# Kernel optimization log

Measured on AMD Instinct MI355X. Metric: run time of the kernel, lower is better.

The kernel has to match this reference:

```python
import jax, jax.numpy as jnp
import numpy as np

K = 3  # n_components (hardcoded in original fit())
NORM = float(np.sqrt((2.0 * np.pi) ** 3))


def _prob(X, mean, dev):
    # X: [N,H,W,3], mean: [K,H,W,3], dev: [K,H,W] -> prob [N,K,H,W]
    d2 = jnp.sum(jnp.square(X[:, None] - mean[None]), axis=-1)  # [N,K,H,W]
    return jnp.exp(-d2 / (2.0 * jnp.square(dev)[None])) / (NORM * dev[None])


def _fit(frames, n_iter):
    N, H, W, _ = frames.shape
    # init: mean[k] = (k+1)/4, deviation = 1, weight = 1/K (as in original)
    mean = jnp.stack([jnp.full((H, W, 3), (k + 1) / 4.0, jnp.float32) for k in range(K)])
    dev = jnp.ones((K, H, W), jnp.float32)
    weight = jnp.full((K, H, W), 1.0 / K, jnp.float32)

    def step(carry, _):
        weight, mean, dev = carry
        P = _prob(frames, mean, dev)                      # [N,K,H,W]
        R = weight[None] * P
        R = R / jnp.sum(R, axis=1, keepdims=True)         # responsibilities
        Rs = jnp.sum(R, axis=0)                           # [K,H,W]
        w = Rs / N
        m = jnp.einsum('nkhw,nhwc->khwc', R, frames) / Rs[..., None]
        d = jnp.sum(R * jnp.sum(jnp.square(frames[:, None] - m[None]), axis=-1), axis=0) / Rs
        return (w, m, d), None

    (weight, mean, dev), _ = jax.lax.scan(step, (weight, mean, dev), None, length=n_iter)
    ratio = weight / dev
    fg = ratio <= jnp.min(ratio, axis=0)                  # [K,H,W] bool
    return weight, mean, dev, fg


def _process(frame, mean, dev, fg):
    # frame: [H,W,3]
    dist = jnp.sqrt(jnp.sum(jnp.square(frame[None] - mean), axis=-1))  # [K,H,W]
    index = jnp.argmin(dist, axis=0)                                   # [H,W]
    min_dist = jnp.min(dist, axis=0)                                   # [H,W]
    dev_c = jnp.take_along_axis(dev, index[None], axis=0)[0]
    mask1 = min_dist < dev_c * 2.5
    mask2 = jnp.take_along_axis(fg, index[None], axis=0)[0]
    _ = jnp.logical_and(mask1, mask2)  # computed but unused in original return
    # channel 0: original return (mask2 * 255); channel 1: min_dist (differentiable core)
    return jnp.stack([mask2.astype(jnp.float32) * 255.0, min_dist], axis=0)


def setup_inputs() -> dict:
    key = jax.random.key(0)
    k1, k2 = jax.random.split(key)
    frames = jax.random.uniform(k1, (8, 480, 640, 3), dtype=jnp.float32)
    frame = jax.random.uniform(k2, (480, 640, 3), dtype=jnp.float32)
    return {"frames": frames, "frame": frame, "n_iter": 5}


def reference(frames, frame, n_iter):
    weight, mean, dev, fg = _fit(frames, n_iter)
    return _process(frame, mean, dev, fg)
```

## Files before the change

kernel.cpp:

```cpp
#include <hip/hip_runtime.h>
#include <math.h>

#define KC 3
#define NF 8
#define NPJ 4
#define HH 480
#define WW 640
#define HWPIX (HH * WW)
#define FSTRIDE (HWPIX * 3)

typedef float v2f __attribute__((ext_vector_type(2)));

__device__ __forceinline__ float frcp(float x) { return __builtin_amdgcn_rcpf(x); }
__device__ __forceinline__ float fexp2(float x) { return __builtin_amdgcn_exp2f(x); }
__device__ __forceinline__ v2f exp2v(v2f x) { return (v2f){fexp2(x.x), fexp2(x.y)}; }
__device__ __forceinline__ v2f v2(float s) { return (v2f){s, s}; }

__global__ __launch_bounds__(64, 4) void gmm_fit_process_kernel(
    const float* __restrict__ frames,
    const float* __restrict__ frame,
    const int* __restrict__ n_iter_p,
    float* __restrict__ out)
{
    const int p = blockIdx.x * blockDim.x + threadIdx.x;
    if (p >= HWPIX) return;
    const int n_iter = *n_iter_p;

    v2f Xp[NPJ][3], X2p[NPJ];
#pragma unroll
    for (int j = 0; j < NPJ; ++j) {
        const float* s0 = frames + (size_t)(2 * j)     * FSTRIDE + (size_t)p * 3;
        const float* s1 = frames + (size_t)(2 * j + 1) * FSTRIDE + (size_t)p * 3;
        Xp[j][0] = (v2f){s0[0], s1[0]};
        Xp[j][1] = (v2f){s0[1], s1[1]};
        Xp[j][2] = (v2f){s0[2], s1[2]};
        X2p[j] = Xp[j][0] * Xp[j][0] + Xp[j][1] * Xp[j][1] + Xp[j][2] * Xp[j][2];
    }

    float mean[KC][3], dev[KC], weight[KC];
#pragma unroll
    for (int k = 0; k < KC; ++k) {
        const float m0 = (float)(k + 1) / 4.0f;
        mean[k][0] = m0; mean[k][1] = m0; mean[k][2] = m0;
        dev[k] = 1.0f;
        weight[k] = 1.0f / 3.0f;
    }

    const float INV_NORM = 0.06349363593424097f;
    const float L2E = 1.4426950408889634f;
    const float DEV_FLOOR = 1e-12f;
    const float S_FLOOR = 1e-20f;

    for (int it = 0; it < n_iter; ++it) {
        float A[KC], B[KC], C[KC], cc[KC];
#pragma unroll
        for (int k = 0; k < KC; ++k) {
            const float invd = frcp(fmaxf(dev[k], DEV_FLOOR));
            const float a2 = -0.5f * L2E * invd * invd;
            const float m2 = mean[k][0] * mean[k][0] + mean[k][1] * mean[k][1]
                           + mean[k][2] * mean[k][2];
            A[k] = a2;
            B[k] = a2 * m2;
            C[k] = -2.0f * a2;
            cc[k] = weight[k] * INV_NORM * invd;
        }

        v2f rs[KC], mx[KC], my[KC], mz[KC], ac2[KC];
#pragma unroll
        for (int k = 0; k < KC; ++k) {
            rs[k] = v2(0.0f); mx[k] = v2(0.0f); my[k] = v2(0.0f);
            mz[k] = v2(0.0f); ac2[k] = v2(0.0f);
        }

#pragma unroll
        for (int j = 0; j < NPJ; ++j) {
            v2f r[KC], s = v2(0.0f);
#pragma unroll
            for (int k = 0; k < KC; ++k) {
                const v2f t = v2(mean[k][0]) * Xp[j][0]
                            + v2(mean[k][1]) * Xp[j][1]
                            + v2(mean[k][2]) * Xp[j][2];
                v2f e = v2(A[k]) * X2p[j] + v2(B[k]);
                e = v2(C[k]) * t + e;
                r[k] = v2(cc[k]) * exp2v(e);
                s += r[k];
            }
            const v2f sinv = (v2f){ (s.x > S_FLOOR) ? frcp(s.x) : 0.0f,
                                    (s.y > S_FLOOR) ? frcp(s.y) : 0.0f };
#pragma unroll
            for (int k = 0; k < KC; ++k) {
                const v2f rk = r[k] * sinv;
                rs[k]  += rk;
                mx[k]  += rk * Xp[j][0];
                my[k]  += rk * Xp[j][1];
                mz[k]  += rk * Xp[j][2];
                ac2[k] += rk * X2p[j];
            }
        }

#pragma unroll
        for (int k = 0; k < KC; ++k) {
            const float rsk = rs[k].x + rs[k].y;
            const float mxs = mx[k].x + mx[k].y;
            const float mys = my[k].x + my[k].y;
            const float mzs = mz[k].x + mz[k].y;
            const float a2s = ac2[k].x + ac2[k].y;
            const float invrs = frcp(rsk);
            const float nm0 = mxs * invrs, nm1 = mys * invrs, nm2 = mzs * invrs;
            const float mm2 = nm0 * nm0 + nm1 * nm1 + nm2 * nm2;
            const float ndev = a2s * invrs - mm2;
            const bool ok = rsk > S_FLOOR;
            mean[k][0] = ok ? nm0 : mean[k][0];
            mean[k][1] = ok ? nm1 : mean[k][1];
            mean[k][2] = ok ? nm2 : mean[k][2];
            dev[k]     = ok ? ndev : dev[k];
            weight[k]  = rsk * 0.125f;
        }
    }

    float ratio[KC];
    float rmin = 3.402823466e+38f;
#pragma unroll
    for (int k = 0; k < KC; ++k) {
        ratio[k] = weight[k] * frcp(fmaxf(dev[k], DEV_FLOOR));
        rmin = fminf(rmin, ratio[k]);
    }

    const float fx = frame[(size_t)p * 3 + 0];
    const float fy = frame[(size_t)p * 3 + 1];
    const float fz = frame[(size_t)p * 3 + 2];

    float mind = 3.402823466e+38f;
    int index = 0;
#pragma unroll
    for (int k = 0; k < KC; ++k) {
        const float dx = fx - mean[k][0];
        const float dy = fy - mean[k][1];
        const float dz = fz - mean[k][2];
        const float dist = __builtin_amdgcn_sqrtf(dx * dx + dy * dy + dz * dz);
        if (dist < mind) { mind = dist; index = k; }
    }

    const float mask = (ratio[index] <= rmin) ? 255.0f : 0.0f;
    out[p] = mask;
    out[HWPIX + p] = isfinite(mind) ? mind : 0.0f;
}

extern "C" void kernel_launch(void* const* d_in, const int* in_sizes, int n_in,
                              void* d_out, int out_size, void* d_ws, size_t ws_size,
                              hipStream_t stream) {
    const float* frames = (const float*)d_in[0];
    const float* frame  = (const float*)d_in[1];
    const int*   n_iter = (const int*)d_in[2];
    float* out = (float*)d_out;

    const int threads = 64;
    const int blocks = (HWPIX + threads - 1) / threads;
    gmm_fit_process_kernel<<<blocks, threads, 0, stream>>>(frames, frame, n_iter, out);
}
```

Measured before the change: 23.83 us.

## Split each pixel's frames across two lanes with DPP pair reduction

Each pixel is now handled by two adjacent lanes, each owning four of the eight frames. Per-iteration sufficient statistics are combined with a DPP quad-permute pair sum, and frames are reloaded from memory each iteration instead of being held in registers. This doubles thread count and lifts the occupancy hint, trading extra global reloads for lower register pressure and more latency hiding. It also drops the normalisation constant, which cancels in the responsibilities, and folds the exponent into fewer operations.

After: 73.93 us. 3.1x slower.

```diff
diff --git a/kernel.cpp b/kernel.cpp
--- a/kernel.cpp
+++ b/kernel.cpp
@@ -2,8 +2,6 @@
 #include <math.h>
 
 #define KC 3
-#define NF 8
-#define NPJ 4
 #define HH 480
 #define WW 640
 #define HWPIX (HH * WW)
@@ -16,26 +14,21 @@
 __device__ __forceinline__ v2f exp2v(v2f x) { return (v2f){fexp2(x.x), fexp2(x.y)}; }
 __device__ __forceinline__ v2f v2(float s) { return (v2f){s, s}; }
 
-__global__ __launch_bounds__(64, 4) void gmm_fit_process_kernel(
+__device__ __forceinline__ float dpp_pair_sum(float x) {
+    int v = __builtin_amdgcn_update_dpp(0, __float_as_int(x), 0xB1, 0xF, 0xF, true);
+    return x + __int_as_float(v);
+}
+
+__global__ __launch_bounds__(64, 8) void gmm_fit_process_kernel(
     const float* __restrict__ frames,
     const float* __restrict__ frame,
     const int* __restrict__ n_iter_p,
     float* __restrict__ out)
 {
-    const int p = blockIdx.x * blockDim.x + threadIdx.x;
-    if (p >= HWPIX) return;
+    const int t = blockIdx.x * 64 + threadIdx.x;
+    const int p = t >> 1;
+    const int h = t & 1;
     const int n_iter = *n_iter_p;
-
-    v2f Xp[NPJ][3], X2p[NPJ];
-#pragma unroll
-    for (int j = 0; j < NPJ; ++j) {
-        const float* s0 = frames + (size_t)(2 * j)     * FSTRIDE + (size_t)p * 3;
-        const float* s1 = frames + (size_t)(2 * j + 1) * FSTRIDE + (size_t)p * 3;
-        Xp[j][0] = (v2f){s0[0], s1[0]};
-        Xp[j][1] = (v2f){s0[1], s1[1]};
-        Xp[j][2] = (v2f){s0[2], s1[2]};
-        X2p[j] = Xp[j][0] * Xp[j][0] + Xp[j][1] * Xp[j][1] + Xp[j][2] * Xp[j][2];
-    }
 
     float mean[KC][3], dev[KC], weight[KC];
 #pragma unroll
@@ -46,13 +39,14 @@
         weight[k] = 1.0f / 3.0f;
     }
 
-    const float INV_NORM = 0.06349363593424097f;
     const float L2E = 1.4426950408889634f;
     const float DEV_FLOOR = 1e-12f;
     const float S_FLOOR = 1e-20f;
 
+    const float* my_base = frames + (size_t)(4 * h) * FSTRIDE + (size_t)p * 3;
+
     for (int it = 0; it < n_iter; ++it) {
-        float A[KC], B[KC], C[KC], cc[KC];
+        float A[KC], B[KC], cc[KC];
 #pragma unroll
         for (int k = 0; k < KC; ++k) {
             const float invd = frcp(fmaxf(dev[k], DEV_FLOOR));
@@ -61,27 +55,29 @@
                            + mean[k][2] * mean[k][2];
             A[k] = a2;
             B[k] = a2 * m2;
-            C[k] = -2.0f * a2;
-            cc[k] = weight[k] * INV_NORM * invd;
+            cc[k] = weight[k] * invd;
         }
 
-        v2f rs[KC], mx[KC], my[KC], mz[KC], ac2[KC];
+        float rs[KC], mx[KC], my[KC], mz[KC], ac2[KC];
 #pragma unroll
-        for (int k = 0; k < KC; ++k) {
-            rs[k] = v2(0.0f); mx[k] = v2(0.0f); my[k] = v2(0.0f);
-            mz[k] = v2(0.0f); ac2[k] = v2(0.0f);
-        }
+        for (int k = 0; k < KC; ++k) { rs[k] = mx[k] = my[k] = mz[k] = ac2[k] = 0.0f; }
 
 #pragma unroll
-        for (int j = 0; j < NPJ; ++j) {
+        for (int j = 0; j < 2; ++j) {
+            const float* a = my_base + (size_t)(2 * j) * FSTRIDE;
+            const float* b = a + FSTRIDE;
+            const v2f x0 = (v2f){a[0], b[0]};
+            const v2f x1 = (v2f){a[1], b[1]};
+            const v2f x2 = (v2f){a[2], b[2]};
+            const v2f q = x0 * x0 + x1 * x1 + x2 * x2;
+
             v2f r[KC], s = v2(0.0f);
 #pragma unroll
             for (int k = 0; k < KC; ++k) {
-                const v2f t = v2(mean[k][0]) * Xp[j][0]
-                            + v2(mean[k][1]) * Xp[j][1]
-                            + v2(mean[k][2]) * Xp[j][2];
-                v2f e = v2(A[k]) * X2p[j] + v2(B[k]);
-                e = v2(C[k]) * t + e;
+                const v2f td = v2(mean[k][0]) * x0 + v2(mean[k][1]) * x1
+                             + v2(mean[k][2]) * x2;
+                const v2f u = q - v2(2.0f) * td;
+                const v2f e = v2(A[k]) * u + v2(B[k]);
                 r[k] = v2(cc[k]) * exp2v(e);
                 s += r[k];
             }
@@ -90,31 +86,39 @@
 #pragma unroll
             for (int k = 0; k < KC; ++k) {
                 const v2f rk = r[k] * sinv;
-                rs[k]  += rk;
-                mx[k]  += rk * Xp[j][0];
-                my[k]  += rk * Xp[j][1];
-                mz[k]  += rk * Xp[j][2];
-                ac2[k] += rk * X2p[j];
+                const v2f c0 = rk * x0;
+                const v2f c1 = rk * x1;
+                const v2f c2 = rk * x2;
+                const v2f cq = rk * q;
+                rs[k]  += rk.x;  rs[k]  += rk.y;
+                mx[k]  += c0.x;  mx[k]  += c0.y;
+                my[k]  += c1.x;  my[k]  += c1.y;
+                mz[k]  += c2.x;  mz[k]  += c2.y;
+                ac2[k] += cq.x;  ac2[k] += cq.y;
             }
         }
 
 #pragma unroll
         for (int k = 0; k < KC; ++k) {
-            const float rsk = rs[k].x + rs[k].y;
-            const float mxs = mx[k].x + mx[k].y;
-            const float mys = my[k].x + my[k].y;
-            const float mzs = mz[k].x + mz[k].y;
-            const float a2s = ac2[k].x + ac2[k].y;
-            const float invrs = frcp(rsk);
-            const float nm0 = mxs * invrs, nm1 = mys * invrs, nm2 = mzs * invrs;
+            rs[k]  = dpp_pair_sum(rs[k]);
+            mx[k]  = dpp_pair_sum(mx[k]);
+            my[k]  = dpp_pair_sum(my[k]);
+            mz[k]  = dpp_pair_sum(mz[k]);
+            ac2[k] = dpp_pair_sum(ac2[k]);
+        }
+
+#pragma unroll
+        for (int k = 0; k < KC; ++k) {
+            const float invrs = frcp(rs[k]);
+            const float nm0 = mx[k] * invrs, nm1 = my[k] * invrs, nm2 = mz[k] * invrs;
             const float mm2 = nm0 * nm0 + nm1 * nm1 + nm2 * nm2;
-            const float ndev = a2s * invrs - mm2;
-            const bool ok = rsk > S_FLOOR;
+            const float ndev = ac2[k] * invrs - mm2;
+            const bool ok = rs[k] > S_FLOOR;
             mean[k][0] = ok ? nm0 : mean[k][0];
             mean[k][1] = ok ? nm1 : mean[k][1];
             mean[k][2] = ok ? nm2 : mean[k][2];
             dev[k]     = ok ? ndev : dev[k];
-            weight[k]  = rsk * 0.125f;
+            weight[k]  = rs[k] * 0.125f;
         }
     }
 
@@ -126,9 +130,8 @@
         rmin = fminf(rmin, ratio[k]);
     }
 
-    const float fx = frame[(size_t)p * 3 + 0];
-    const float fy = frame[(size_t)p * 3 + 1];
-    const float fz = frame[(size_t)p * 3 + 2];
+    const float* fr = frame + (size_t)p * 3;
+    const float fx = fr[0], fy = fr[1], fz = fr[2];
 
     float mind = 3.402823466e+38f;
     int index = 0;
@@ -142,8 +145,10 @@
     }
 
     const float mask = (ratio[index] <= rmin) ? 255.0f : 0.0f;
-    out[p] = mask;
-    out[HWPIX + p] = isfinite(mind) ? mind : 0.0f;
+    const float md = isfinite(mind) ? mind : 0.0f;
+
+    const float val = h ? md : mask;
+    out[(size_t)h * HWPIX + p] = val;
 }
 
 extern "C" void kernel_launch(void* const* d_in, const int* in_sizes, int n_in,
@@ -155,6 +160,6 @@
     float* out = (float*)d_out;
 
     const int threads = 64;
-    const int blocks = (HWPIX + threads - 1) / threads;
+    const int blocks = (HWPIX * 2) / threads;
     gmm_fit_process_kernel<<<blocks, threads, 0, stream>>>(frames, frame, n_iter, out);
 }
```
